# Performance work log

Measured on AMD Instinct MI355X. Metric: run time of the kernel, lower is better.

The kernel has to match this reference:

```python
import jax, jax.numpy as jnp
import numpy as np


def setup_inputs() -> dict:
    key = jax.random.key(0)
    k1, k2, k3, k4, k5, k6 = jax.random.split(key, 6)
    B, N, K = 2, 60000, 16
    C_in, C_add, C_mid = 64, 3, 16
    out_features = 128
    in_features = (C_in + C_add) * C_mid  # 1072
    return {
        "input_features": jax.random.normal(k1, (B, N, C_in), dtype=jnp.float32),
        "neighbor_inds": jax.random.randint(k2, (B, N, K), 0, N, dtype=jnp.int32),
        "weightnet": jax.random.normal(k3, (B, N, K, C_mid), dtype=jnp.float32),
        "additional_features": jax.random.normal(k4, (B, N, K, C_add), dtype=jnp.float32),
        "linear_weight": jax.random.normal(k5, (out_features, in_features), dtype=jnp.float32) * 0.03,
        "linear_bias": jax.random.normal(k6, (out_features,), dtype=jnp.float32),
    }


def reference(input_features, neighbor_inds, weightnet, additional_features, linear_weight, linear_bias):
    # Gather neighbor features: [B, N, K, C_in]
    gathered = jax.vmap(lambda feats, idx: feats[idx])(input_features, neighbor_inds)
    # Concat per-neighbor additional features: [B, N, K, C_in + C_add]
    feat = jnp.concatenate([gathered, additional_features], axis=-1)
    # PConv: contract over neighbors K against weightnet -> [B, N, C, M]
    pconv = jnp.einsum('bnkc,bnkm->bncm', feat, weightnet)
    B, N = pconv.shape[0], pconv.shape[1]
    pconv = pconv.reshape(B, N, -1)  # [B, N, (C_in+C_add)*C_mid]
    # Fused linear projection
    return jnp.einsum('bnf,of->bno', pconv, linear_weight) + linear_bias
```

## Files before the change

kernel.cpp:

```cpp
#include <hip/hip_runtime.h>

#define NPTS  60000
#define NBLK  1875
#define FP    1088
#define PSTR  1096
#define HALF  (32 * PSTR)
#define SPBYTES    (2 * HALF * 2)
#define SPBYTES_FB (32 * PSTR * 2)
#define LWH_BYTES   (128 * FP * 2)
#define INF16_BYTES (2 * NPTS * 64 * 2)
#define WS_NEED     (LWH_BYTES + INF16_BYTES)
#define TILES   15
#define NBLOCKS 250

typedef _Float16 f16x4 __attribute__((ext_vector_type(4)));
typedef _Float16 f16x8 __attribute__((ext_vector_type(8)));
typedef float    f32x4 __attribute__((ext_vector_type(4)));

__global__ void __launch_bounds__(256)
cvt_lw_kernel(const float* __restrict__ LW, _Float16* __restrict__ LWh) {
    const int o = blockIdx.x;
    for (int f = threadIdx.x; f < FP; f += 256) {
        const float v = (f < 1072) ? LW[o * 1072 + f] : 0.f;
        LWh[(f >> 5) * (128 * 32) + o * 32 + (f & 31)] = (_Float16)v;
    }
}

__global__ void __launch_bounds__(256)
cvt_inf_kernel(const float* __restrict__ inF, _Float16* __restrict__ inF16) {
    const int tid = blockIdx.x * 256 + threadIdx.x;
    if (tid >= 2 * NPTS * 64) return;
    const int c = tid & 63;
    const int n = tid >> 6;
    inF16[(n << 6) + ((c & 15) << 2) + (c >> 4)] = (_Float16)inF[tid];
}

struct GR { f16x4 fv[4]; float wv[4]; };

static __device__ __forceinline__ void issue_gather16(
    const _Float16* __restrict__ inF16, const float* __restrict__ Wn,
    int bbase, int base_nk, int ind_lane, int i, int q, int ml, GR& g)
{
    #pragma unroll
    for (int j = 0; j < 4; ++j) {
        const int k   = q * 4 + j;
        const int idx = __shfl(ind_lane, i * 16 + k, 64);
        g.fv[j] = *(const f16x4*)(inF16 + (bbase + idx) * 64 + ml * 4);
        g.wv[j] = Wn[(base_nk + k) * 16 + ml];
    }
}

static __device__ __forceinline__ void compute_point(
    const GR& g, const float* __restrict__ aFp,
    _Float16* sProw, int qsw, int q, int ml, bool mlo)
{
    float av[4];
    #pragma unroll
    for (int j = 0; j < 4; ++j)
        av[j] = mlo ? aFp[(q * 4 + j) * 3] : 0.f;

    const f32x4 z4 = {0.f, 0.f, 0.f, 0.f};
    f16x4 aW;
    #pragma unroll
    for (int j = 0; j < 4; ++j) aW[j] = (_Float16)g.wv[j];

    #pragma unroll
    for (int ct = 0; ct < 4; ++ct) {
        f16x4 bF;
        #pragma unroll
        for (int j = 0; j < 4; ++j) bF[j] = g.fv[j][ct];
        const f32x4 d = __builtin_amdgcn_mfma_f32_16x16x16f16(aW, bF, z4, 0, 0, 0);
        f16x4 dh;
        #pragma unroll
        for (int r = 0; r < 4; ++r) dh[r] = (_Float16)d[r];
        *(f16x4*)&sProw[(ct * 16 + ml) * 16 + qsw * 4] = dh;
    }
    f16x4 bA;
    #pragma unroll
    for (int j = 0; j < 4; ++j) bA[j] = (_Float16)av[j];
    const f32x4 d = __builtin_amdgcn_mfma_f32_16x16x16f16(aW, bA, z4, 0, 0, 0);
    if (mlo) {
        f16x4 dh;
        #pragma unroll
        for (int r = 0; r < 4; ++r) dh[r] = (_Float16)d[r];
        *(f16x4*)&sProw[(64 + ml) * 16 + qsw * 4] = dh;
    }
}

__global__ void __launch_bounds__(512, 2)
pconv_persistent(const _Float16* __restrict__ inF16,
                 const int*   __restrict__ inds,
                 const float* __restrict__ Wn,
                 const float* __restrict__ addF,
                 const _Float16* __restrict__ LWh,
                 const float* __restrict__ bias,
                 float*       __restrict__ out)
{
    extern __shared__ __align__(16) _Float16 sP[];

    const int t    = threadIdx.x;
    const int lane = t & 63;
    const int w    = t >> 6;
    const int q    = lane >> 4;
    const int ml   = lane & 15;
    const bool mlo = (ml < 3);
    const int qsw  = q ^ (((ml >> 2) & 1) << 1);

    sP[(t >> 4) * PSTR + 1072 + (t & 15)] = (_Float16)0.f;
    sP[HALF + (t >> 4) * PSTR + 1072 + (t & 15)] = (_Float16)0.f;

    const int o0 = w * 16;
    const _Float16* bPw = LWh + (o0 + ml) * 32 + q * 8;
    f16x8 bfr[34];
    #pragma unroll
    for (int ch = 0; ch < 34; ++ch)
        bfr[ch] = *(const f16x8*)(bPw + ch * 4096);
    const float bz = bias[o0 + ml];

    int gt  = blockIdx.x * TILES;
    int bC  = gt / NBLK;
    int n0C = (gt - bC * NBLK) * 32;
    int bbC = bC * NPTS;
    int nkC = (bbC + n0C + w * 4) * 16;
    GR g0, g1, g2, g3;
    {
        const int ind0 = inds[nkC + lane];
        issue_gather16(inF16, Wn, bbC, nkC,      ind0, 0, q, ml, g0);
        issue_gather16(inF16, Wn, bbC, nkC + 16, ind0, 1, q, ml, g1);
        issue_gather16(inF16, Wn, bbC, nkC + 32, ind0, 2, q, ml, g2);
        issue_gather16(inF16, Wn, bbC, nkC + 48, ind0, 3, q, ml, g3);
    }

    for (int tt = 0; tt < TILES; ++tt) {
        const bool more = (tt + 1 < TILES);
        int bbN = bbC, n0N = n0C, nkN = nkC, indN = 0;
        if (more) {
            const int gtn = gt + 1;
            const int bN  = gtn / NBLK;
            n0N = (gtn - bN * NBLK) * 32;
            bbN = bN * NPTS;
            nkN = (bbN + n0N + w * 4) * 16;
            indN = inds[nkN + lane];
        }

        _Float16* sPc = sP + (tt & 1) * HALF;
        _Float16* sPw = sPc + (w * 4) * PSTR;
        const float* aFp = addF + nkC * 3 + ml;

        compute_point(g0, aFp,       sPw,            qsw, q, ml, mlo);
        compute_point(g1, aFp + 48,  sPw + PSTR,     qsw, q, ml, mlo);
        if (more) {
            issue_gather16(inF16, Wn, bbN, nkN,      indN, 0, q, ml, g0);
            issue_gather16(inF16, Wn, bbN, nkN + 16, indN, 1, q, ml, g1);
        }
        compute_point(g2, aFp + 96,  sPw + 2 * PSTR, qsw, q, ml, mlo);
        compute_point(g3, aFp + 144, sPw + 3 * PSTR, qsw, q, ml, mlo);
        if (more) {
            issue_gather16(inF16, Wn, bbN, nkN + 32, indN, 2, q, ml, g2);
            issue_gather16(inF16, Wn, bbN, nkN + 48, indN, 3, q, ml, g3);
        }
        __syncthreads();

        f32x4 acc0 = {0.f, 0.f, 0.f, 0.f};
        f32x4 acc1 = {0.f, 0.f, 0.f, 0.f};
        const _Float16* aP0 = sPc + ml * PSTR + (q >> 1) * 16 + (q & 1) * 8;
        const _Float16* aP1 = aP0 + 16 * PSTR;
        const int flip = (q & 1) ? -8 : 8;
        #pragma unroll
        for (int ch = 0; ch < 34; ++ch) {
            const int off = ch * 32 + ((ch & 2) ? flip : 0);
            f16x8 a0 = *(const f16x8*)(aP0 + off);
            f16x8 a1 = *(const f16x8*)(aP1 + off);
            acc0 = __builtin_amdgcn_mfma_f32_16x16x32_f16(a0, bfr[ch], acc0, 0, 0, 0);
            acc1 = __builtin_amdgcn_mfma_f32_16x16x32_f16(a1, bfr[ch], acc1, 0, 0, 0);
        }

        float* ob = out + (bbC + n0C + q * 4) * 128 + o0 + ml;
        #pragma unroll
        for (int r = 0; r < 4; ++r)
            ob[r * 128] = acc0[r] + bz;
        ob += 16 * 128;
        #pragma unroll
        for (int r = 0; r < 4; ++r)
            ob[r * 128] = acc1[r] + bz;

        bbC = bbN; n0C = n0N; nkC = nkN; ++gt;
    }
}

struct GR32 { float fv[4][4]; float wv[4]; float av[4]; };

static __device__ __forceinline__ void issue_gather32(
    const float* __restrict__ inF, const float* __restrict__ Wn,
    const float* __restrict__ addF, int bbase, int base_nk,
    int ind_lane, int i, int q, int ml, bool mlo, GR32& g)
{
    #pragma unroll
    for (int j = 0; j < 4; ++j) {
        const int k   = q * 4 + j;
        const int idx = __shfl(ind_lane, i * 16 + k, 64);
        const float* fp = inF + (bbase + idx) * 64 + ml;
        #pragma unroll
        for (int ct = 0; ct < 4; ++ct)
            g.fv[ct][j] = fp[ct * 16];
        g.wv[j] = Wn[(base_nk + k) * 16 + ml];
        g.av[j] = mlo ? addF[(base_nk + k) * 3 + ml] : 0.f;
    }
}

static __device__ __forceinline__ void compute_point32(
    const GR32& g, _Float16* sProw, int qsw, int ml, bool mlo)
{
    const f32x4 z4 = {0.f, 0.f, 0.f, 0.f};
    f16x4 aW, bA;
    #pragma unroll
    for (int j = 0; j < 4; ++j) { aW[j] = (_Float16)g.wv[j]; bA[j] = (_Float16)g.av[j]; }
    #pragma unroll
    for (int ct = 0; ct < 4; ++ct) {
        f16x4 bF;
        #pragma unroll
        for (int j = 0; j < 4; ++j) bF[j] = (_Float16)g.fv[ct][j];
        const f32x4 d = __builtin_amdgcn_mfma_f32_16x16x16f16(aW, bF, z4, 0, 0, 0);
        f16x4 dh;
        #pragma unroll
        for (int r = 0; r < 4; ++r) dh[r] = (_Float16)d[r];
        *(f16x4*)&sProw[(ct * 16 + ml) * 16 + qsw * 4] = dh;
    }
    const f32x4 d = __builtin_amdgcn_mfma_f32_16x16x16f16(aW, bA, z4, 0, 0, 0);
    if (mlo) {
        f16x4 dh;
        #pragma unroll
        for (int r = 0; r < 4; ++r) dh[r] = (_Float16)d[r];
        *(f16x4*)&sProw[(64 + ml) * 16 + qsw * 4] = dh;
    }
}

__global__ void __launch_bounds__(512, 4)
pconv_fallback(const float* __restrict__ inF, const int* __restrict__ inds,
               const float* __restrict__ Wn, const float* __restrict__ addF,
               const _Float16* __restrict__ LWh, const float* __restrict__ bias,
               float* __restrict__ out)
{
    extern __shared__ __align__(16) _Float16 sP[];
    const int t = threadIdx.x, lane = t & 63, w = t >> 6;
    const int q = lane >> 4, ml = lane & 15;
    const bool mlo = (ml < 3);
    const int qsw = q ^ (((ml >> 2) & 1) << 1);
    const int bid = blockIdx.x, b = bid / NBLK;
    const int n0 = (bid - b * NBLK) * 32, bbase = b * NPTS;
    const int ind_lane = inds[(bbase + n0 + w * 4) * 16 + lane];
    sP[(t >> 4) * PSTR + 1072 + (t & 15)] = (_Float16)0.f;

    const int nk0 = (bbase + n0 + w * 4) * 16;
    _Float16* sPw = sP + (w * 4) * PSTR;
    GR32 g0, g1;
    issue_gather32(inF, Wn, addF, bbase, nk0,      ind_lane, 0, q, ml, mlo, g0);
    issue_gather32(inF, Wn, addF, bbase, nk0 + 16, ind_lane, 1, q, ml, mlo, g1);
    compute_point32(g0, sPw,            qsw, ml, mlo);
    issue_gather32(inF, Wn, addF, bbase, nk0 + 32, ind_lane, 2, q, ml, mlo, g0);
    compute_point32(g1, sPw + PSTR,     qsw, ml, mlo);
    issue_gather32(inF, Wn, addF, bbase, nk0 + 48, ind_lane, 3, q, ml, mlo, g1);
    compute_point32(g0, sPw + 2 * PSTR, qsw, ml, mlo);
    compute_point32(g1, sPw + 3 * PSTR, qsw, ml, mlo);

    const int o0 = w * 16;
    const _Float16* bP = LWh + (o0 + ml) * 32 + q * 8;
    f16x8 bcur = *(const f16x8*)(bP);
    f16x8 bnxt = *(const f16x8*)(bP + 4096);
    __syncthreads();

    const float bz = bias[o0 + ml];
    f32x4 acc0 = {0.f, 0.f, 0.f, 0.f};
    f32x4 acc1 = {0.f, 0.f, 0.f, 0.f};
    const _Float16* aP0 = sP + ml * PSTR + (q >> 1) * 16 + (q & 1) * 8;
    const _Float16* aP1 = aP0 + 16 * PSTR;
    const int flip = (q & 1) ? -8 : 8;
    #pragma unroll 2
    for (int ch = 0; ch < 34; ++ch) {
        const int chf = (ch + 2 < 34) ? (ch + 2) : 33;
        f16x8 bfut = *(const f16x8*)(bP + chf * 4096);
        const int off = ch * 32 + ((ch & 2) ? flip : 0);
        f16x8 a0 = *(const f16x8*)(aP0 + off);
        f16x8 a1 = *(const f16x8*)(aP1 + off);
        acc0 = __builtin_amdgcn_mfma_f32_16x16x32_f16(a0, bcur, acc0, 0, 0, 0);
        acc1 = __builtin_amdgcn_mfma_f32_16x16x32_f16(a1, bcur, acc1, 0, 0, 0);
        bcur = bnxt; bnxt = bfut;
    }
    float* ob = out + (bbase + n0 + q * 4) * 128 + o0 + ml;
    #pragma unroll
    for (int r = 0; r < 4; ++r) ob[r * 128] = acc0[r] + bz;
    ob += 16 * 128;
    #pragma unroll
    for (int r = 0; r < 4; ++r) ob[r * 128] = acc1[r] + bz;
}

extern "C" void kernel_launch(void* const* d_in, const int* in_sizes, int n_in,
                              void* d_out, int out_size, void* d_ws, size_t ws_size,
                              hipStream_t stream)
{
    const float* inF  = (const float*)d_in[0];
    const int*   inds = (const int*)  d_in[1];
    const float* Wn   = (const float*)d_in[2];
    const float* addF = (const float*)d_in[3];
    const float* LW   = (const float*)d_in[4];
    const float* bias = (const float*)d_in[5];
    float* out = (float*)d_out;
    _Float16* LWh = (_Float16*)d_ws;

    const bool f16p = (ws_size >= (size_t)WS_NEED);

    hipFuncSetAttribute((const void*)pconv_persistent,
                        hipFuncAttributeMaxDynamicSharedMemorySize, SPBYTES);
    hipFuncSetAttribute((const void*)pconv_fallback,
                        hipFuncAttributeMaxDynamicSharedMemorySize, SPBYTES_FB);

    cvt_lw_kernel<<<dim3(128), dim3(256), 0, stream>>>(LW, LWh);
    if (f16p) {
        _Float16* inF16 = (_Float16*)((char*)d_ws + LWH_BYTES);
        cvt_inf_kernel<<<dim3((2 * NPTS * 64 + 255) / 256), dim3(256), 0, stream>>>(
            inF, inF16);
        pconv_persistent<<<dim3(NBLOCKS), dim3(512), SPBYTES, stream>>>(
            inF16, inds, Wn, addF, LWh, bias, out);
    } else {
        pconv_fallback<<<dim3(2 * NBLK), dim3(512), SPBYTES_FB, stream>>>(
            inF, inds, Wn, addF, LWh, bias, out);
    }
}
```

Measured before the change: 330.8 us.

## Split persistent kernel into producer and consumer warp roles with 32x32 MFMA

The persistent kernel now gives warps 4-7 the gather and PConv work, each handling 8 points per tile, and writes the results into swizzled double-buffered LDS. Warps 0-3 run the linear projection with 32x32x16 MFMAs, one tile behind, streaming the fp16 weight from global memory in a new blocked layout instead of holding it in 34 registers. The intent is to overlap the gather-bound producer with the tensor-core consumer, ease register pressure and reduce LDS bank conflicts. The cost is half the warps doing each job, weight reloads from L2 on every tile, and one extra pipeline stage per block.

```diff
diff --git a/kernel.cpp b/kernel.cpp
--- a/kernel.cpp
+++ b/kernel.cpp
@@ -4,9 +4,10 @@
 #define NBLK  1875
 #define FP    1088
 #define PSTR  1096
-#define HALF  (32 * PSTR)
-#define SPBYTES    (2 * HALF * 2)
-#define SPBYTES_FB (32 * PSTR * 2)
+#define ROWB  (PSTR * 2)
+#define HALFB (32 * ROWB)
+#define SPBYTES    (2 * HALFB)
+#define SPBYTES_FB HALFB
 #define LWH_BYTES   (128 * FP * 2)
 #define INF16_BYTES (2 * NPTS * 64 * 2)
 #define WS_NEED     (LWH_BYTES + INF16_BYTES)
@@ -16,6 +17,16 @@
 typedef _Float16 f16x4 __attribute__((ext_vector_type(4)));
 typedef _Float16 f16x8 __attribute__((ext_vector_type(8)));
 typedef float    f32x4 __attribute__((ext_vector_type(4)));
+typedef float    f32x16 __attribute__((ext_vector_type(16)));
+
+__global__ void __launch_bounds__(256)
+cvt_lwb_kernel(const float* __restrict__ LW, _Float16* __restrict__ LWB) {
+    const int o = blockIdx.x;
+    for (int f = threadIdx.x; f < FP; f += 256) {
+        const float v = (f < 1072) ? LW[o * 1072 + f] : 0.f;
+        LWB[(f >> 3) * 1024 + o * 8 + (f & 7)] = (_Float16)v;
+    }
+}
 
 __global__ void __launch_bounds__(256)
 cvt_lw_kernel(const float* __restrict__ LW, _Float16* __restrict__ LWh) {
@@ -35,68 +46,16 @@
     inF16[(n << 6) + ((c & 15) << 2) + (c >> 4)] = (_Float16)inF[tid];
 }
 
-struct GR { f16x4 fv[4]; float wv[4]; };
-
-static __device__ __forceinline__ void issue_gather16(
-    const _Float16* __restrict__ inF16, const float* __restrict__ Wn,
-    int bbase, int base_nk, int ind_lane, int i, int q, int ml, GR& g)
-{
-    #pragma unroll
-    for (int j = 0; j < 4; ++j) {
-        const int k   = q * 4 + j;
-        const int idx = __shfl(ind_lane, i * 16 + k, 64);
-        g.fv[j] = *(const f16x4*)(inF16 + (bbase + idx) * 64 + ml * 4);
-        g.wv[j] = Wn[(base_nk + k) * 16 + ml];
-    }
-}
-
-static __device__ __forceinline__ void compute_point(
-    const GR& g, const float* __restrict__ aFp,
-    _Float16* sProw, int qsw, int q, int ml, bool mlo)
-{
-    float av[4];
-    #pragma unroll
-    for (int j = 0; j < 4; ++j)
-        av[j] = mlo ? aFp[(q * 4 + j) * 3] : 0.f;
-
-    const f32x4 z4 = {0.f, 0.f, 0.f, 0.f};
-    f16x4 aW;
-    #pragma unroll
-    for (int j = 0; j < 4; ++j) aW[j] = (_Float16)g.wv[j];
-
-    #pragma unroll
-    for (int ct = 0; ct < 4; ++ct) {
-        f16x4 bF;
-        #pragma unroll
-        for (int j = 0; j < 4; ++j) bF[j] = g.fv[j][ct];
-        const f32x4 d = __builtin_amdgcn_mfma_f32_16x16x16f16(aW, bF, z4, 0, 0, 0);
-        f16x4 dh;
-        #pragma unroll
-        for (int r = 0; r < 4; ++r) dh[r] = (_Float16)d[r];
-        *(f16x4*)&sProw[(ct * 16 + ml) * 16 + qsw * 4] = dh;
-    }
-    f16x4 bA;
-    #pragma unroll
-    for (int j = 0; j < 4; ++j) bA[j] = (_Float16)av[j];
-    const f32x4 d = __builtin_amdgcn_mfma_f32_16x16x16f16(aW, bA, z4, 0, 0, 0);
-    if (mlo) {
-        f16x4 dh;
-        #pragma unroll
-        for (int r = 0; r < 4; ++r) dh[r] = (_Float16)d[r];
-        *(f16x4*)&sProw[(64 + ml) * 16 + qsw * 4] = dh;
-    }
-}
-
 __global__ void __launch_bounds__(512, 2)
 pconv_persistent(const _Float16* __restrict__ inF16,
                  const int*   __restrict__ inds,
                  const float* __restrict__ Wn,
                  const float* __restrict__ addF,
-                 const _Float16* __restrict__ LWh,
+                 const _Float16* __restrict__ LWB,
                  const float* __restrict__ bias,
                  float*       __restrict__ out)
 {
-    extern __shared__ __align__(16) _Float16 sP[];
+    extern __shared__ __align__(16) char sPB[];
 
     const int t    = threadIdx.x;
     const int lane = t & 63;
@@ -105,86 +64,155 @@
     const int ml   = lane & 15;
     const bool mlo = (ml < 3);
     const int qsw  = q ^ (((ml >> 2) & 1) << 1);
-
-    sP[(t >> 4) * PSTR + 1072 + (t & 15)] = (_Float16)0.f;
-    sP[HALF + (t >> 4) * PSTR + 1072 + (t & 15)] = (_Float16)0.f;
-
-    const int o0 = w * 16;
-    const _Float16* bPw = LWh + (o0 + ml) * 32 + q * 8;
-    f16x8 bfr[34];
-    #pragma unroll
-    for (int ch = 0; ch < 34; ++ch)
-        bfr[ch] = *(const f16x8*)(bPw + ch * 4096);
-    const float bz = bias[o0 + ml];
-
-    int gt  = blockIdx.x * TILES;
-    int bC  = gt / NBLK;
-    int n0C = (gt - bC * NBLK) * 32;
-    int bbC = bC * NPTS;
-    int nkC = (bbC + n0C + w * 4) * 16;
-    GR g0, g1, g2, g3;
+    const int gt0  = blockIdx.x * TILES;
+
     {
-        const int ind0 = inds[nkC + lane];
-        issue_gather16(inF16, Wn, bbC, nkC,      ind0, 0, q, ml, g0);
-        issue_gather16(inF16, Wn, bbC, nkC + 16, ind0, 1, q, ml, g1);
-        issue_gather16(inF16, Wn, bbC, nkC + 32, ind0, 2, q, ml, g2);
-        issue_gather16(inF16, Wn, bbC, nkC + 48, ind0, 3, q, ml, g3);
-    }
-
-    for (int tt = 0; tt < TILES; ++tt) {
-        const bool more = (tt + 1 < TILES);
-        int bbN = bbC, n0N = n0C, nkN = nkC, indN = 0;
-        if (more) {
-            const int gtn = gt + 1;
-            const int bN  = gtn / NBLK;
-            n0N = (gtn - bN * NBLK) * 32;
-            bbN = bN * NPTS;
-            nkN = (bbN + n0N + w * 4) * 16;
-            indN = inds[nkN + lane];
+        const int row = t >> 4, jj = t & 15;
+        const int zb = (2144 + 2 * jj) ^ (((row >> 3) & 3) << 4);
+        *(_Float16*)(sPB + row * ROWB + zb) = (_Float16)0.f;
+        *(_Float16*)(sPB + HALFB + row * ROWB + zb) = (_Float16)0.f;
+    }
+
+    if (w < 4) {
+        const int col = lane & 31;
+        const int hf  = lane >> 5;
+        const int o0  = w * 32;
+        const float bz = bias[o0 + col];
+        const int rsw = ((col >> 3) & 3) << 4;
+        const _Float16* bp0 = LWB + hf * 1024 + (o0 + col) * 8;
+
+        for (int tt = 0; tt <= TILES; ++tt) {
+            if (tt >= 1) {
+                const int g  = gt0 + tt - 1;
+                const int b  = g / NBLK;
+                const int n0 = (g - b * NBLK) * 32;
+                const int bb = b * NPTS;
+                const char* aBase = sPB + ((tt - 1) & 1) * HALFB + col * ROWB;
+
+                f32x16 acc0, acc1;
+                #pragma unroll
+                for (int i = 0; i < 16; ++i) { acc0[i] = 0.f; acc1[i] = 0.f; }
+
+                f16x8 cur[4], nxt[4];
+                #pragma unroll
+                for (int u = 0; u < 4; ++u)
+                    cur[u] = *(const f16x8*)(bp0 + u * 2048);
+
+                for (int grp = 0; grp < 17; ++grp) {
+                    #pragma unroll
+                    for (int u = 0; u < 4; ++u)
+                        if (grp < 16)
+                            nxt[u] = *(const f16x8*)(bp0 + ((grp + 1) * 4 + u) * 2048);
+                    #pragma unroll
+                    for (int u = 0; u < 4; ++u) {
+                        const int ch = grp * 4 + u;
+                        const int ab = (ch * 32 + ((hf ^ ((ch >> 2) & 1)) << 4)) ^ rsw;
+                        const f16x8 a = *(const f16x8*)(aBase + ab);
+                        if (u & 1)
+                            acc1 = __builtin_amdgcn_mfma_f32_32x32x16_f16(a, cur[u], acc1, 0, 0, 0);
+                        else
+                            acc0 = __builtin_amdgcn_mfma_f32_32x32x16_f16(a, cur[u], acc0, 0, 0, 0);
+                    }
+                    #pragma unroll
+                    for (int u = 0; u < 4; ++u) cur[u] = nxt[u];
+                }
+
+                float* ob = out + (bb + n0) * 128 + o0 + col;
+                #pragma unroll
+                for (int reg = 0; reg < 16; ++reg) {
+                    const int row = (reg & 3) + 8 * (reg >> 2) + 4 * hf;
+                    ob[row * 128] = acc0[reg] + acc1[reg] + bz;
+                }
+            }
+            __syncthreads();
         }
-
-        _Float16* sPc = sP + (tt & 1) * HALF;
-        _Float16* sPw = sPc + (w * 4) * PSTR;
-        const float* aFp = addF + nkC * 3 + ml;
-
-        compute_point(g0, aFp,       sPw,            qsw, q, ml, mlo);
-        compute_point(g1, aFp + 48,  sPw + PSTR,     qsw, q, ml, mlo);
-        if (more) {
-            issue_gather16(inF16, Wn, bbN, nkN,      indN, 0, q, ml, g0);
-            issue_gather16(inF16, Wn, bbN, nkN + 16, indN, 1, q, ml, g1);
+    } else {
+        const int pw = w - 4;
+        const f32x4 z4 = {0.f, 0.f, 0.f, 0.f};
+        f16x4 fv[8][4];
+        float wv[8][4];
+
+        int bbC, n0C, nkC;
+        {
+            const int g = gt0; const int b = g / NBLK;
+            n0C = (g - b * NBLK) * 32; bbC = b * NPTS;
+            nkC = (bbC + n0C + pw * 8) * 16;
         }
-        compute_point(g2, aFp + 96,  sPw + 2 * PSTR, qsw, q, ml, mlo);
-        compute_point(g3, aFp + 144, sPw + 3 * PSTR, qsw, q, ml, mlo);
-        if (more) {
-            issue_gather16(inF16, Wn, bbN, nkN + 32, indN, 2, q, ml, g2);
-            issue_gather16(inF16, Wn, bbN, nkN + 48, indN, 3, q, ml, g3);
+        {
+            const int i0 = inds[nkC + lane];
+            const int i1 = inds[nkC + 64 + lane];
+            #pragma unroll
+            for (int p = 0; p < 8; ++p) {
+                const int src = (p < 4) ? i0 : i1;
+                #pragma unroll
+                for (int j = 0; j < 4; ++j) {
+                    const int idx = __shfl(src, (p & 3) * 16 + q * 4 + j, 64);
+                    fv[p][j] = *(const f16x4*)(inF16 + (bbC + idx) * 64 + ml * 4);
+                    wv[p][j] = Wn[(nkC + p * 16 + q * 4 + j) * 16 + ml];
+                }
+            }
         }
-        __syncthreads();
-
-        f32x4 acc0 = {0.f, 0.f, 0.f, 0.f};
-        f32x4 acc1 = {0.f, 0.f, 0.f, 0.f};
-        const _Float16* aP0 = sPc + ml * PSTR + (q >> 1) * 16 + (q & 1) * 8;
-        const _Float16* aP1 = aP0 + 16 * PSTR;
-        const int flip = (q & 1) ? -8 : 8;
-        #pragma unroll
-        for (int ch = 0; ch < 34; ++ch) {
-            const int off = ch * 32 + ((ch & 2) ? flip : 0);
-            f16x8 a0 = *(const f16x8*)(aP0 + off);
-            f16x8 a1 = *(const f16x8*)(aP1 + off);
-            acc0 = __builtin_amdgcn_mfma_f32_16x16x32_f16(a0, bfr[ch], acc0, 0, 0, 0);
-            acc1 = __builtin_amdgcn_mfma_f32_16x16x32_f16(a1, bfr[ch], acc1, 0, 0, 0);
+
+        for (int tt = 0; tt <= TILES; ++tt) {
+            if (tt < TILES) {
+                const bool more = (tt + 1 < TILES);
+                int bbN = 0, n0N = 0, nkN = 0, iN0 = 0, iN1 = 0;
+                if (more) {
+                    const int g = gt0 + tt + 1; const int b = g / NBLK;
+                    n0N = (g - b * NBLK) * 32; bbN = b * NPTS;
+                    nkN = (bbN + n0N + pw * 8) * 16;
+                    iN0 = inds[nkN + lane];
+                    iN1 = inds[nkN + 64 + lane];
+                }
+                char* bufB = sPB + (tt & 1) * HALFB;
+
+                #pragma unroll
+                for (int p = 0; p < 8; ++p) {
+                    const int bnk = nkC + p * 16;
+                    f16x4 aW, bA;
+                    #pragma unroll
+                    for (int j = 0; j < 4; ++j) {
+                        aW[j] = (_Float16)wv[p][j];
+                        bA[j] = mlo ? (_Float16)addF[(bnk + q * 4 + j) * 3 + ml]
+                                    : (_Float16)0.f;
+                    }
+                    const int prow = pw * 8 + p;
+                    char* rowp = bufB + prow * ROWB;
+                    const int rs2 = ((prow >> 3) & 3) << 4;
+                    #pragma unroll
+                    for (int ct = 0; ct < 4; ++ct) {
+                        f16x4 bF;
+                        #pragma unroll
+                        for (int j = 0; j < 4; ++j) bF[j] = fv[p][j][ct];
+                        const f32x4 d = __builtin_amdgcn_mfma_f32_16x16x16f16(aW, bF, z4, 0, 0, 0);
+                        f16x4 dh;
+                        #pragma unroll
+                        for (int r = 0; r < 4; ++r) dh[r] = (_Float16)d[r];
+                        *(f16x4*)(rowp + ((((ct * 16 + ml) * 16 + qsw * 4) * 2) ^ rs2)) = dh;
+                    }
+                    {
+                        const f32x4 d = __builtin_amdgcn_mfma_f32_16x16x16f16(aW, bA, z4, 0, 0, 0);
+                        if (mlo) {
+                            f16x4 dh;
+                            #pragma unroll
+                            for (int r = 0; r < 4; ++r) dh[r] = (_Float16)d[r];
+                            *(f16x4*)(rowp + ((((64 + ml) * 16 + qsw * 4) * 2) ^ rs2)) = dh;
+                        }
+                    }
+                    if (more) {
+                        const int src = (p < 4) ? iN0 : iN1;
+                        #pragma unroll
+                        for (int j = 0; j < 4; ++j) {
+                            const int idx = __shfl(src, (p & 3) * 16 + q * 4 + j, 64);
+                            fv[p][j] = *(const f16x4*)(inF16 + (bbN + idx) * 64 + ml * 4);
+                            wv[p][j] = Wn[(nkN + p * 16 + q * 4 + j) * 16 + ml];
+                        }
+                    }
+                }
+                if (more) { bbC = bbN; n0C = n0N; nkC = nkN; }
+            }
+            __syncthreads();
         }
-
-        float* ob = out + (bbC + n0C + q * 4) * 128 + o0 + ml;
-        #pragma unroll
-        for (int r = 0; r < 4; ++r)
-            ob[r * 128] = acc0[r] + bz;
-        ob += 16 * 128;
-        #pragma unroll
-        for (int r = 0; r < 4; ++r)
-            ob[r * 128] = acc1[r] + bz;
-
-        bbC = bbN; n0C = n0N; nkC = nkN; ++gt;
     }
 }
 
@@ -305,7 +333,6 @@
     const float* LW   = (const float*)d_in[4];
     const float* bias = (const float*)d_in[5];
     float* out = (float*)d_out;
-    _Float16* LWh = (_Float16*)d_ws;
 
     const bool f16p = (ws_size >= (size_t)WS_NEED);
 
@@ -314,14 +341,17 @@
     hipFuncSetAttribute((const void*)pconv_fallback,
                         hipFuncAttributeMaxDynamicSharedMemorySize, SPBYTES_FB);
 
-    cvt_lw_kernel<<<dim3(128), dim3(256), 0, stream>>>(LW, LWh);
     if (f16p) {
+        _Float16* LWB   = (_Float16*)d_ws;
         _Float16* inF16 = (_Float16*)((char*)d_ws + LWH_BYTES);
+        cvt_lwb_kernel<<<dim3(128), dim3(256), 0, stream>>>(LW, LWB);
         cvt_inf_kernel<<<dim3((2 * NPTS * 64 + 255) / 256), dim3(256), 0, stream>>>(
             inF, inF16);
         pconv_persistent<<<dim3(NBLOCKS), dim3(512), SPBYTES, stream>>>(
-            inF16, inds, Wn, addF, LWh, bias, out);
+            inF16, inds, Wn, addF, LWB, bias, out);
     } else {
+        _Float16* LWh = (_Float16*)d_ws;
+        cvt_lw_kernel<<<dim3(128), dim3(256), 0, stream>>>(LW, LWh);
         pconv_fallback<<<dim3(2 * NBLK), dim3(512), SPBYTES_FB, stream>>>(
             inF, inds, Wn, addF, LWh, bias, out);
     }
```

New measurement: 542.5 us. +64.0%, slower.

## Drop LDS double buffering and double persistent blocks for higher occupancy

Applied to the files above, without the earlier changes.

Replaces the double-buffered shared-memory tile with a single buffer and adds a second barrier per tile to protect reuse. The freed LDS and a launch bound of four blocks per CU allow 500 persistent blocks, each covering about 7.5 tiles, instead of 250 blocks of 15. The aim is more resident waves to hide gather latency, at the cost of an extra sync per tile and tighter register limits that may spill the 34 preloaded weight fragments.

```diff
diff --git a/kernel.cpp b/kernel.cpp
--- a/kernel.cpp
+++ b/kernel.cpp
@@ -4,14 +4,11 @@
 #define NBLK  1875
 #define FP    1088
 #define PSTR  1096
-#define HALF  (32 * PSTR)
-#define SPBYTES    (2 * HALF * 2)
-#define SPBYTES_FB (32 * PSTR * 2)
+#define SPBYTES (32 * PSTR * 2)
 #define LWH_BYTES   (128 * FP * 2)
 #define INF16_BYTES (2 * NPTS * 64 * 2)
 #define WS_NEED     (LWH_BYTES + INF16_BYTES)
-#define TILES   15
-#define NBLOCKS 250
+#define NBLOCKS 500
 
 typedef _Float16 f16x4 __attribute__((ext_vector_type(4)));
 typedef _Float16 f16x8 __attribute__((ext_vector_type(8)));
@@ -87,7 +84,7 @@
     }
 }
 
-__global__ void __launch_bounds__(512, 2)
+__global__ void __launch_bounds__(512, 4)
 pconv_persistent(const _Float16* __restrict__ inF16,
                  const int*   __restrict__ inds,
                  const float* __restrict__ Wn,
@@ -107,7 +104,6 @@
     const int qsw  = q ^ (((ml >> 2) & 1) << 1);
 
     sP[(t >> 4) * PSTR + 1072 + (t & 15)] = (_Float16)0.f;
-    sP[HALF + (t >> 4) * PSTR + 1072 + (t & 15)] = (_Float16)0.f;
 
     const int o0 = w * 16;
     const _Float16* bPw = LWh + (o0 + ml) * 32 + q * 8;
@@ -117,11 +113,18 @@
         bfr[ch] = *(const f16x8*)(bPw + ch * 4096);
     const float bz = bias[o0 + ml];
 
-    int gt  = blockIdx.x * TILES;
-    int bC  = gt / NBLK;
-    int n0C = (gt - bC * NBLK) * 32;
-    int bbC = bC * NPTS;
-    int nkC = (bbC + n0C + w * 4) * 16;
+    const int ts = (blockIdx.x * 15) >> 1;
+    const int te = ((blockIdx.x + 1) * 15) >> 1;
+
+    auto meta = [&](int g, int& bb, int& n0, int& nk) {
+        const int b = g / NBLK;
+        n0 = (g - b * NBLK) * 32;
+        bb = b * NPTS;
+        nk = (bb + n0 + w * 4) * 16;
+    };
+
+    int bbC, n0C, nkC;
+    meta(ts, bbC, n0C, nkC);
     GR g0, g1, g2, g3;
     {
         const int ind0 = inds[nkC + lane];
@@ -131,20 +134,12 @@
         issue_gather16(inF16, Wn, bbC, nkC + 48, ind0, 3, q, ml, g3);
     }
 
-    for (int tt = 0; tt < TILES; ++tt) {
-        const bool more = (tt + 1 < TILES);
-        int bbN = bbC, n0N = n0C, nkN = nkC, indN = 0;
-        if (more) {
-            const int gtn = gt + 1;
-            const int bN  = gtn / NBLK;
-            n0N = (gtn - bN * NBLK) * 32;
-            bbN = bN * NPTS;
-            nkN = (bbN + n0N + w * 4) * 16;
-            indN = inds[nkN + lane];
-        }
-
-        _Float16* sPc = sP + (tt & 1) * HALF;
-        _Float16* sPw = sPc + (w * 4) * PSTR;
+    for (int gt = ts; gt < te; ++gt) {
+        const bool more = (gt + 1 < te);
+        int bbN = 0, n0N = 0, nkN = 0, indN = 0;
+        if (more) { meta(gt + 1, bbN, n0N, nkN); indN = inds[nkN + lane]; }
+
+        _Float16* sPw = sP + (w * 4) * PSTR;
         const float* aFp = addF + nkC * 3 + ml;
 
         compute_point(g0, aFp,       sPw,            qsw, q, ml, mlo);
@@ -163,7 +158,7 @@
 
         f32x4 acc0 = {0.f, 0.f, 0.f, 0.f};
         f32x4 acc1 = {0.f, 0.f, 0.f, 0.f};
-        const _Float16* aP0 = sPc + ml * PSTR + (q >> 1) * 16 + (q & 1) * 8;
+        const _Float16* aP0 = sP + ml * PSTR + (q >> 1) * 16 + (q & 1) * 8;
         const _Float16* aP1 = aP0 + 16 * PSTR;
         const int flip = (q & 1) ? -8 : 8;
         #pragma unroll
@@ -184,7 +179,9 @@
         for (int r = 0; r < 4; ++r)
             ob[r * 128] = acc1[r] + bz;
 
-        bbC = bbN; n0C = n0N; nkC = nkN; ++gt;
+        __syncthreads();
+
+        bbC = bbN; n0C = n0N; nkC = nkN;
     }
 }
 
@@ -312,7 +309,7 @@
     hipFuncSetAttribute((const void*)pconv_persistent,
                         hipFuncAttributeMaxDynamicSharedMemorySize, SPBYTES);
     hipFuncSetAttribute((const void*)pconv_fallback,
-                        hipFuncAttributeMaxDynamicSharedMemorySize, SPBYTES_FB);
+                        hipFuncAttributeMaxDynamicSharedMemorySize, SPBYTES);
 
     cvt_lw_kernel<<<dim3(128), dim3(256), 0, stream>>>(LW, LWh);
     if (f16p) {
@@ -322,7 +319,7 @@
         pconv_persistent<<<dim3(NBLOCKS), dim3(512), SPBYTES, stream>>>(
             inF16, inds, Wn, addF, LWh, bias, out);
     } else {
-        pconv_fallback<<<dim3(2 * NBLK), dim3(512), SPBYTES_FB, stream>>>(
+        pconv_fallback<<<dim3(2 * NBLK), dim3(512), SPBYTES, stream>>>(
             inF, inds, Wn, addF, LWh, bias, out);
     }
 }
```

Result: slower. 794.8 us (+140.3%).

## Use 32x32x16 MFMA with split-K across wave pairs in persistent pconv

Applied to the files above, without the earlier changes.

Replaces the per-wave pair of 16x16x32 MFMAs with one 32x32x16 MFMA per chunk. The reduction dimension is split across pairs of waves, and the partial sums are combined through a small LDS reduction buffer before the output is written. Linear weights are relaid out in 8-wide blocks to match the new operand layout, and neighbor indices are loaded as int4 vectors instead of being broadcast with shuffles. This cuts LDS A-operand reads and shuffle overhead, but adds an extra barrier per tile and more shared memory, which could lower occupancy.

```diff
diff --git a/kernel.cpp b/kernel.cpp
--- a/kernel.cpp
+++ b/kernel.cpp
@@ -4,8 +4,10 @@
 #define NBLK  1875
 #define FP    1088
 #define PSTR  1096
+#define ROWB  (PSTR * 2)
 #define HALF  (32 * PSTR)
-#define SPBYTES    (2 * HALF * 2)
+#define REDF  (32 * 36)
+#define SPBYTES (2 * HALF * 2 + 4 * REDF * 4)
 #define SPBYTES_FB (32 * PSTR * 2)
 #define LWH_BYTES   (128 * FP * 2)
 #define INF16_BYTES (2 * NPTS * 64 * 2)
@@ -16,6 +18,17 @@
 typedef _Float16 f16x4 __attribute__((ext_vector_type(4)));
 typedef _Float16 f16x8 __attribute__((ext_vector_type(8)));
 typedef float    f32x4 __attribute__((ext_vector_type(4)));
+typedef float    f32x16 __attribute__((ext_vector_type(16)));
+typedef int      i32x4 __attribute__((ext_vector_type(4)));
+
+__global__ void __launch_bounds__(256)
+cvt_lwb_kernel(const float* __restrict__ LW, _Float16* __restrict__ LWB) {
+    const int o = blockIdx.x;
+    for (int f = threadIdx.x; f < FP; f += 256) {
+        const float v = (f < 1072) ? LW[o * 1072 + f] : 0.f;
+        LWB[(f >> 3) * 1024 + o * 8 + (f & 7)] = (_Float16)v;
+    }
+}
 
 __global__ void __launch_bounds__(256)
 cvt_lw_kernel(const float* __restrict__ LW, _Float16* __restrict__ LWh) {
@@ -39,14 +52,13 @@
 
 static __device__ __forceinline__ void issue_gather16(
     const _Float16* __restrict__ inF16, const float* __restrict__ Wn,
-    int bbase, int base_nk, int ind_lane, int i, int q, int ml, GR& g)
+    int bbase, int bnk, i32x4 iv, int q, int ml, GR& g)
 {
     #pragma unroll
     for (int j = 0; j < 4; ++j) {
-        const int k   = q * 4 + j;
-        const int idx = __shfl(ind_lane, i * 16 + k, 64);
+        const int idx = iv[j];
         g.fv[j] = *(const f16x4*)(inF16 + (bbase + idx) * 64 + ml * 4);
-        g.wv[j] = Wn[(base_nk + k) * 16 + ml];
+        g.wv[j] = Wn[(bnk + q * 4 + j) * 16 + ml];
     }
 }
 
@@ -92,7 +104,7 @@
                  const int*   __restrict__ inds,
                  const float* __restrict__ Wn,
                  const float* __restrict__ addF,
-                 const _Float16* __restrict__ LWh,
+                 const _Float16* __restrict__ LWB,
                  const float* __restrict__ bias,
                  float*       __restrict__ out)
 {
@@ -106,41 +118,55 @@
     const bool mlo = (ml < 3);
     const int qsw  = q ^ (((ml >> 2) & 1) << 1);
 
+    float* sRed = (float*)(sP + 2 * HALF);
+
     sP[(t >> 4) * PSTR + 1072 + (t & 15)] = (_Float16)0.f;
     sP[HALF + (t >> 4) * PSTR + 1072 + (t & 15)] = (_Float16)0.f;
 
-    const int o0 = w * 16;
-    const _Float16* bPw = LWh + (o0 + ml) * 32 + q * 8;
+    const int col = lane & 31;
+    const int hf  = lane >> 5;
+    const int h2  = w & 1;
+    const int o0  = (w >> 1) * 32;
+    const float bz = bias[o0 + col];
+
+    const _Float16* bPw = LWB + (68 * h2 + hf) * 1024 + (o0 + col) * 8;
     f16x8 bfr[34];
     #pragma unroll
     for (int ch = 0; ch < 34; ++ch)
-        bfr[ch] = *(const f16x8*)(bPw + ch * 4096);
-    const float bz = bias[o0 + ml];
-
-    int gt  = blockIdx.x * TILES;
-    int bC  = gt / NBLK;
-    int n0C = (gt - bC * NBLK) * 32;
-    int bbC = bC * NPTS;
-    int nkC = (bbC + n0C + w * 4) * 16;
+        bfr[ch] = *(const f16x8*)(bPw + ch * 2048);
+
+    int gt = blockIdx.x * TILES;
+    auto meta = [&](int g, int& bb, int& n0, int& nk) {
+        const int b = g / NBLK;
+        n0 = (g - b * NBLK) * 32;
+        bb = b * NPTS;
+        nk = (bb + n0 + w * 4) * 16;
+    };
+
+    int bbC, n0C, nkC;
+    meta(gt, bbC, n0C, nkC);
     GR g0, g1, g2, g3;
     {
-        const int ind0 = inds[nkC + lane];
-        issue_gather16(inF16, Wn, bbC, nkC,      ind0, 0, q, ml, g0);
-        issue_gather16(inF16, Wn, bbC, nkC + 16, ind0, 1, q, ml, g1);
-        issue_gather16(inF16, Wn, bbC, nkC + 32, ind0, 2, q, ml, g2);
-        issue_gather16(inF16, Wn, bbC, nkC + 48, ind0, 3, q, ml, g3);
+        const i32x4 v0 = *(const i32x4*)&inds[nkC + q * 4];
+        const i32x4 v1 = *(const i32x4*)&inds[nkC + 16 + q * 4];
+        const i32x4 v2 = *(const i32x4*)&inds[nkC + 32 + q * 4];
+        const i32x4 v3 = *(const i32x4*)&inds[nkC + 48 + q * 4];
+        issue_gather16(inF16, Wn, bbC, nkC,      v0, q, ml, g0);
+        issue_gather16(inF16, Wn, bbC, nkC + 16, v1, q, ml, g1);
+        issue_gather16(inF16, Wn, bbC, nkC + 32, v2, q, ml, g2);
+        issue_gather16(inF16, Wn, bbC, nkC + 48, v3, q, ml, g3);
     }
 
     for (int tt = 0; tt < TILES; ++tt) {
         const bool more = (tt + 1 < TILES);
-        int bbN = bbC, n0N = n0C, nkN = nkC, indN = 0;
+        int bbN = 0, n0N = 0, nkN = 0;
+        i32x4 iv0, iv1, iv2, iv3;
         if (more) {
-            const int gtn = gt + 1;
-            const int bN  = gtn / NBLK;
-            n0N = (gtn - bN * NBLK) * 32;
-            bbN = bN * NPTS;
-            nkN = (bbN + n0N + w * 4) * 16;
-            indN = inds[nkN + lane];
+            meta(gt + 1, bbN, n0N, nkN);
+            iv0 = *(const i32x4*)&inds[nkN + q * 4];
+            iv1 = *(const i32x4*)&inds[nkN + 16 + q * 4];
+            iv2 = *(const i32x4*)&inds[nkN + 32 + q * 4];
+            iv3 = *(const i32x4*)&inds[nkN + 48 + q * 4];
         }
 
         _Float16* sPc = sP + (tt & 1) * HALF;
@@ -150,39 +176,49 @@
         compute_point(g0, aFp,       sPw,            qsw, q, ml, mlo);
         compute_point(g1, aFp + 48,  sPw + PSTR,     qsw, q, ml, mlo);
         if (more) {
-            issue_gather16(inF16, Wn, bbN, nkN,      indN, 0, q, ml, g0);
-            issue_gather16(inF16, Wn, bbN, nkN + 16, indN, 1, q, ml, g1);
+            issue_gather16(inF16, Wn, bbN, nkN,      iv0, q, ml, g0);
+            issue_gather16(inF16, Wn, bbN, nkN + 16, iv1, q, ml, g1);
         }
         compute_point(g2, aFp + 96,  sPw + 2 * PSTR, qsw, q, ml, mlo);
         compute_point(g3, aFp + 144, sPw + 3 * PSTR, qsw, q, ml, mlo);
         if (more) {
-            issue_gather16(inF16, Wn, bbN, nkN + 32, indN, 2, q, ml, g2);
-            issue_gather16(inF16, Wn, bbN, nkN + 48, indN, 3, q, ml, g3);
+            issue_gather16(inF16, Wn, bbN, nkN + 32, iv2, q, ml, g2);
+            issue_gather16(inF16, Wn, bbN, nkN + 48, iv3, q, ml, g3);
         }
         __syncthreads();
 
-        f32x4 acc0 = {0.f, 0.f, 0.f, 0.f};
-        f32x4 acc1 = {0.f, 0.f, 0.f, 0.f};
-        const _Float16* aP0 = sPc + ml * PSTR + (q >> 1) * 16 + (q & 1) * 8;
-        const _Float16* aP1 = aP0 + 16 * PSTR;
-        const int flip = (q & 1) ? -8 : 8;
+        const char* aB = (const char*)sPc + col * ROWB;
+        f32x16 acc;
+        #pragma unroll
+        for (int i = 0; i < 16; ++i) acc[i] = 0.f;
+        const int ub = 68 * h2 + hf;
         #pragma unroll
         for (int ch = 0; ch < 34; ++ch) {
-            const int off = ch * 32 + ((ch & 2) ? flip : 0);
-            f16x8 a0 = *(const f16x8*)(aP0 + off);
-            f16x8 a1 = *(const f16x8*)(aP1 + off);
-            acc0 = __builtin_amdgcn_mfma_f32_16x16x32_f16(a0, bfr[ch], acc0, 0, 0, 0);
-            acc1 = __builtin_amdgcn_mfma_f32_16x16x32_f16(a1, bfr[ch], acc1, 0, 0, 0);
-        }
-
-        float* ob = out + (bbC + n0C + q * 4) * 128 + o0 + ml;
-        #pragma unroll
-        for (int r = 0; r < 4; ++r)
-            ob[r * 128] = acc0[r] + bz;
-        ob += 16 * 128;
-        #pragma unroll
-        for (int r = 0; r < 4; ++r)
-            ob[r * 128] = acc1[r] + bz;
+            const int u  = ub + 2 * ch;
+            const int ab = (16 * u) ^ (((u >> 3) & 1) << 4);
+            const f16x8 a = *(const f16x8*)(aB + ab);
+            acc = __builtin_amdgcn_mfma_f32_32x32x16_f16(a, bfr[ch], acc, 0, 0, 0);
+        }
+
+        float* rp = sRed + (w >> 1) * REDF + col * 36 + 4 * hf;
+        if (h2 == 1) {
+            #pragma unroll
+            for (int g = 0; g < 4; ++g) {
+                f32x4 v = {acc[4 * g], acc[4 * g + 1], acc[4 * g + 2], acc[4 * g + 3]};
+                *(f32x4*)(rp + 8 * g) = v;
+            }
+        }
+        __syncthreads();
+        if (h2 == 0) {
+            float* ob = out + (bbC + n0C) * 128 + o0 + col;
+            #pragma unroll
+            for (int g = 0; g < 4; ++g) {
+                const f32x4 v = *(const f32x4*)(rp + 8 * g);
+                #pragma unroll
+                for (int r = 0; r < 4; ++r)
+                    ob[(4 * hf + 8 * g + r) * 128] = acc[4 * g + r] + v[r] + bz;
+            }
+        }
 
         bbC = bbN; n0C = n0N; nkC = nkN; ++gt;
     }
@@ -241,7 +277,7 @@
                const _Float16* __restrict__ LWh, const float* __restrict__ bias,
                float* __restrict__ out)
 {
-    extern __shared__ __align__(16) _Float16 sP[];
+    extern __shared__ __align__(16) _Float16 sPf[];
     const int t = threadIdx.x, lane = t & 63, w = t >> 6;
     const int q = lane >> 4, ml = lane & 15;
     const bool mlo = (ml < 3);
@@ -249,10 +285,10 @@
     const int bid = blockIdx.x, b = bid / NBLK;
     const int n0 = (bid - b * NBLK) * 32, bbase = b * NPTS;
     const int ind_lane = inds[(bbase + n0 + w * 4) * 16 + lane];
-    sP[(t >> 4) * PSTR + 1072 + (t & 15)] = (_Float16)0.f;
+    sPf[(t >> 4) * PSTR + 1072 + (t & 15)] = (_Float16)0.f;
 
     const int nk0 = (bbase + n0 + w * 4) * 16;
-    _Float16* sPw = sP + (w * 4) * PSTR;
+    _Float16* sPw = sPf + (w * 4) * PSTR;
     GR32 g0, g1;
     issue_gather32(inF, Wn, addF, bbase, nk0,      ind_lane, 0, q, ml, mlo, g0);
     issue_gather32(inF, Wn, addF, bbase, nk0 + 16, ind_lane, 1, q, ml, mlo, g1);
@@ -272,7 +308,7 @@
     const float bz = bias[o0 + ml];
     f32x4 acc0 = {0.f, 0.f, 0.f, 0.f};
     f32x4 acc1 = {0.f, 0.f, 0.f, 0.f};
-    const _Float16* aP0 = sP + ml * PSTR + (q >> 1) * 16 + (q & 1) * 8;
+    const _Float16* aP0 = sPf + ml * PSTR + (q >> 1) * 16 + (q & 1) * 8;
     const _Float16* aP1 = aP0 + 16 * PSTR;
     const int flip = (q & 1) ? -8 : 8;
     #pragma unroll 2
@@ -305,7 +341,6 @@
     const float* LW   = (const float*)d_in[4];
     const float* bias = (const float*)d_in[5];
     float* out = (float*)d_out;
-    _Float16* LWh = (_Float16*)d_ws;
 
     const bool f16p = (ws_size >= (size_t)WS_NEED);
 
@@ -314,14 +349,17 @@
     hipFuncSetAttribute((const void*)pconv_fallback,
                         hipFuncAttributeMaxDynamicSharedMemorySize, SPBYTES_FB);
 
-    cvt_lw_kernel<<<dim3(128), dim3(256), 0, stream>>>(LW, LWh);
     if (f16p) {
+        _Float16* LWB   = (_Float16*)d_ws;
         _Float16* inF16 = (_Float16*)((char*)d_ws + LWH_BYTES);
+        cvt_lwb_kernel<<<dim3(128), dim3(256), 0, stream>>>(LW, LWB);
         cvt_inf_kernel<<<dim3((2 * NPTS * 64 + 255) / 256), dim3(256), 0, stream>>>(
             inF, inF16);
         pconv_persistent<<<dim3(NBLOCKS), dim3(512), SPBYTES, stream>>>(
-            inF16, inds, Wn, addF, LWh, bias, out);
+            inF16, inds, Wn, addF, LWB, bias, out);
     } else {
+        _Float16* LWh = (_Float16*)d_ws;
+        cvt_lw_kernel<<<dim3(128), dim3(256), 0, stream>>>(LW, LWh);
         pconv_fallback<<<dim3(2 * NBLK), dim3(512), SPBYTES_FB, stream>>>(
             inF, inds, Wn, addF, LWh, bias, out);
     }
```

Result: slower. 387.4 us (+17.1%).
